# Performance work log

Hardware: AMD Instinct MI355X
Metric: run time of the kernel (lower is better)

The kernel has to match this reference:

```python
import jax, jax.numpy as jnp
import numpy as np


def setup_inputs() -> dict:
    key = jax.random.key(0)
    ks = jax.random.split(key, 6)
    B, H, W, Cin, Cout, wdim = 8, 64, 64, 512, 512, 512
    return {
        "x": jax.random.normal(ks[0], (B, H, W, Cin), jnp.float32),
        "w": jax.random.normal(ks[1], (B, wdim), jnp.float32),
        "noise": jax.random.normal(ks[2], (B, H, W, 1), jnp.float32),
        "style_weight": jax.random.normal(ks[3], (wdim, Cin), jnp.float32),
        "style_bias": jnp.ones((Cin,), jnp.float32),
        "conv_weight": jax.random.normal(ks[4], (3, 3, Cin, Cout), jnp.float32),
        "scale_noise": 0.1 * jax.random.normal(ks[5], (1, 1, 1, Cout), jnp.float32),
        "bias": jax.random.normal(jax.random.fold_in(key, 7), (Cout,), jnp.float32),
    }


def reference(x, w, noise, style_weight, style_bias, conv_weight, scale_noise, bias):
    wdim = style_weight.shape[0]
    kh, kw, cin, cout = conv_weight.shape
    # Equalized-LR fully connected to_style (gain=1, lr_mult=1, bias init ones,
    # activation=True -> leaky_relu(0.2) with sqrt(2) gain, StyleGAN2 convention).
    s = w @ (style_weight * (1.0 / np.sqrt(wdim))) + style_bias  # [B, Cin]
    s = jax.nn.leaky_relu(s, 0.2) * np.sqrt(2.0).astype(np.float32)
    # Modulated conv (demodulated). Equalized-LR weight scale 1/sqrt(fan_in).
    wk = conv_weight * (1.0 / np.sqrt(kh * kw * cin))  # [3,3,Cin,Cout]
    # demod[b,o] = rsqrt(sum_{h,w,i} (wk[h,w,i,o]*s[b,i])^2 + eps)
    d = jax.lax.rsqrt(jnp.einsum('hwio,bi->bo', wk * wk, s * s) + 1e-8)  # [B,Cout]
    xm = x * s[:, None, None, :]  # modulate inputs instead of per-sample weights
    y = jax.lax.conv_general_dilated(
        xm, wk, window_strides=(1, 1), padding='SAME',
        dimension_numbers=('NHWC', 'HWIO', 'NHWC'))
    y = y * d[:, None, None, :]
    # noise scale-add + bias + leaky-relu (the fused tail in StyleGAN2 kernels)
    y = y + scale_noise * noise + bias
    return jax.nn.leaky_relu(y, 0.2)
```

## Files before the change

### kernel.cpp

```cpp
#include <hip/hip_runtime.h>
#include <hip/hip_bf16.h>
#include <stdint.h>


typedef __attribute__((ext_vector_type(8))) __bf16 bf16x8;
typedef __attribute__((ext_vector_type(16))) float f32x16;

__device__ __forceinline__ float bf2f(ushort u) {
    union { uint32_t i; float f; } v; v.i = (uint32_t)u << 16; return v.f;
}
__device__ __forceinline__ ushort f2bf(float f) {
    union { float f; uint32_t i; } v; v.f = f;
    uint32_t r = v.i + 0x7fffu + ((v.i >> 16) & 1u);
    return (ushort)(r >> 16);
}
__device__ __forceinline__ int sniff_f32(const void* sb) {
    return ((const uint32_t*)sb)[0] == 0x3F800000u;
}
__device__ __forceinline__ float lda(const void* p, int idx, int isf) {
    return isf ? ((const float*)p)[idx] : bf2f(((const ushort*)p)[idx]);
}

union U16x8 { uint4 v; ushort u[8]; };

#define INV_SQRT_WDIM 0.04419417382415922f
#define SQRT2         1.4142135623730951f
#define WSCALE        0.014731391274719739f

__global__ void k_style_part(const void* __restrict__ w, const void* __restrict__ sw,
                             const void* __restrict__ sb, float* __restrict__ part) {
    int isf = sniff_f32(sb);
    int b = blockIdx.x >> 3, ds = blockIdx.x & 7;
    int i = threadIdx.x;
    __shared__ float wrow[64];
    if (i < 64) wrow[i] = lda(w, b * 512 + ds * 64 + i, isf);
    __syncthreads();
    float acc = 0.f;
    if (isf) {
        const float* p = (const float*)sw + (size_t)ds * 64 * 512;
#pragma unroll 8
        for (int d = 0; d < 64; ++d) acc += wrow[d] * p[d * 512 + i];
    } else {
        const ushort* p = (const ushort*)sw + (size_t)ds * 64 * 512;
#pragma unroll 8
        for (int d = 0; d < 64; ++d) acc += wrow[d] * bf2f(p[d * 512 + i]);
    }
    part[(b * 8 + ds) * 512 + i] = acc;
}

__global__ void k_style_fin(const float* __restrict__ part, const void* __restrict__ sb,
                            float* __restrict__ s_out) {
    int isf = sniff_f32(sb);
    int b = blockIdx.x, i = threadIdx.x;
    float a = 0.f;
#pragma unroll
    for (int ds = 0; ds < 8; ++ds) a += part[(b * 8 + ds) * 512 + i];
    float s = a * INV_SQRT_WDIM + lda(sb, i, isf);
    s = (s > 0.f ? s : 0.2f * s) * SQRT2;
    s_out[b * 512 + i] = s;
}

__global__ void k_pad(const void* __restrict__ x, const float* __restrict__ s,
                      const void* __restrict__ sb, ushort* __restrict__ xmp) {
    int isf = sniff_f32(sb);
    int pr = blockIdx.x;
    int b = pr / 66, yp = pr % 66;
    int tid = threadIdx.x;
    ushort* rowp = xmp + ((size_t)b * 66 + yp) * 66 * 512;
    uint4 z = {0u, 0u, 0u, 0u};
    if (yp == 0 || yp == 65) {
        uint4* p = (uint4*)rowp;
        for (int l = tid; l < 66 * 512 * 2 / 16; l += 256) p[l] = z;
        return;
    }
    __shared__ float sv[512];
    for (int c = tid; c < 512; c += 256) sv[c] = s[b * 512 + c];
    if (tid < 64)       ((uint4*)rowp)[tid] = z;
    else if (tid < 128) ((uint4*)(rowp + 65 * 512))[tid - 64] = z;
    __syncthreads();
    int y = yp - 1;
    ushort* xout = rowp + 512;
    if (isf) {
        const float* xin = (const float*)x + ((size_t)b * 64 + y) * 64 * 512;
        for (int l = tid; l < 8192; l += 256) {
            int xi = l >> 7, cc = (l & 127) * 4;
            float4 in = *(const float4*)(xin + (size_t)xi * 512 + cc);
            ushort4 ov;
            ov.x = f2bf(in.x * sv[cc + 0]);
            ov.y = f2bf(in.y * sv[cc + 1]);
            ov.z = f2bf(in.z * sv[cc + 2]);
            ov.w = f2bf(in.w * sv[cc + 3]);
            *(ushort4*)(xout + (size_t)xi * 512 + cc) = ov;
        }
    } else {
        const ushort* xin = (const ushort*)x + ((size_t)b * 64 + y) * 64 * 512;
        for (int l = tid; l < 4096; l += 256) {
            int xi = l >> 6, cc = (l & 63) * 8;
            U16x8 in, ov;
            in.v = *(const uint4*)(xin + (size_t)xi * 512 + cc);
#pragma unroll
            for (int j = 0; j < 8; ++j) ov.u[j] = f2bf(bf2f(in.u[j]) * sv[cc + j]);
            *(uint4*)(xout + (size_t)xi * 512 + cc) = ov.v;
        }
    }
}

__global__ void k_wt(const void* __restrict__ cw, const void* __restrict__ sb,
                     ushort* __restrict__ wkt) {
    int isf = sniff_f32(sb);
    int bid = blockIdx.x;
    int t = bid / 64, ib = (bid % 64) / 8, ob = bid % 8;
    __shared__ ushort tile[64][65];
    int tid = threadIdx.x;
    int oq = tid & 15, ir = tid >> 4;
#pragma unroll
    for (int p = 0; p < 4; ++p) {
        int i = p * 16 + ir;
        size_t off = ((size_t)(t * 512 + ib * 64 + i)) * 512 + ob * 64 + oq * 4;
        float v0, v1, v2, v3;
        if (isf) {
            float4 v = *(const float4*)((const float*)cw + off);
            v0 = v.x; v1 = v.y; v2 = v.z; v3 = v.w;
        } else {
            ushort4 v = *(const ushort4*)((const ushort*)cw + off);
            v0 = bf2f(v.x); v1 = bf2f(v.y); v2 = bf2f(v.z); v3 = bf2f(v.w);
        }
        tile[i][oq * 4 + 0] = f2bf(v0 * WSCALE);
        tile[i][oq * 4 + 1] = f2bf(v1 * WSCALE);
        tile[i][oq * 4 + 2] = f2bf(v2 * WSCALE);
        tile[i][oq * 4 + 3] = f2bf(v3 * WSCALE);
    }
    __syncthreads();
    int iq = tid & 15, orow = tid >> 4;
#pragma unroll
    for (int p = 0; p < 4; ++p) {
        int o = p * 16 + orow;
        ushort4 v;
        v.x = tile[iq * 4 + 0][o];
        v.y = tile[iq * 4 + 1][o];
        v.z = tile[iq * 4 + 2][o];
        v.w = tile[iq * 4 + 3][o];
        *(ushort4*)(wkt + ((size_t)(t * 512 + ob * 64 + o)) * 512 + ib * 64 + iq * 4) = v;
    }
}

__global__ void k_dmod(const ushort* __restrict__ wkt, const float* __restrict__ s,
                       float* __restrict__ part) {
    int t = blockIdx.x / 8, ob = blockIdx.x % 8;
    int tid = threadIdx.x;
    __shared__ float s2[4096];
    __shared__ float red[2048];
#pragma unroll
    for (int j = 0; j < 16; ++j) {
        int idx = j * 256 + tid;
        float v = s[idx];
        s2[idx] = v * v;
    }
    __syncthreads();
    int ol = tid >> 2, ks = tid & 3;
    int o = ob * 64 + ol;
    const ushort* row = wkt + (size_t)(t * 512 + o) * 512 + ks * 128;
    float acc[8] = {0, 0, 0, 0, 0, 0, 0, 0};
    for (int ch = 0; ch < 16; ++ch) {
        U16x8 wv; wv.v = *(const uint4*)(row + ch * 8);
        int ibase = ks * 128 + ch * 8;
#pragma unroll
        for (int e = 0; e < 8; ++e) {
            float wf = bf2f(wv.u[e]);
            float w2 = wf * wf;
#pragma unroll
            for (int b = 0; b < 8; ++b) acc[b] += w2 * s2[b * 512 + ibase + e];
        }
    }
#pragma unroll
    for (int b = 0; b < 8; ++b) red[(ol * 8 + b) * 4 + ks] = acc[b];
    __syncthreads();
#pragma unroll
    for (int p = 0; p < 2; ++p) {
        int q = tid * 2 + p;
        int ol2 = q >> 3, b2 = q & 7;
        float sum = red[q * 4 + 0] + red[q * 4 + 1] + red[q * 4 + 2] + red[q * 4 + 3];
        part[(b2 * 9 + t) * 512 + ob * 64 + ol2] = sum;
    }
}

__global__ void k_dfin(const float* __restrict__ part, float* __restrict__ d) {
    int gid = blockIdx.x * 256 + threadIdx.x;
    int b = gid >> 9, o = gid & 511;
    float acc = 1e-8f;
#pragma unroll
    for (int t = 0; t < 9; ++t) acc += part[(b * 9 + t) * 512 + o];
    d[b * 512 + o] = rsqrtf(acc);
}

#define GLL(gp, lp) __builtin_amdgcn_global_load_lds( \
    (const __attribute__((address_space(1))) void*)(gp), \
    (__attribute__((address_space(3))) void*)(lp), 16, 0, 0)

__launch_bounds__(256, 2)
__global__ void k_conv(const ushort* __restrict__ xmp, const ushort* __restrict__ wkt,
                       const float* __restrict__ dmod, const void* __restrict__ noise,
                       const void* __restrict__ snoise, const void* __restrict__ bias_,
                       const void* __restrict__ sb, void* __restrict__ out) {
    __shared__ ushort Ah[4 * 66 * 64];
    __shared__ ushort Bl[2][128 * 64];
    int isf = sniff_f32(sb);
    int id = blockIdx.x;
    int ct = id & 3;
    int rt = (id >> 2) & 31;
    int b  = id >> 7;
    int y0 = rt * 2, o0 = ct * 128;
    int tid = threadIdx.x;
    int lane = tid & 63, wv = tid >> 6;
    int wm = (wv >> 1) * 64, wn = (wv & 1) * 64;
    int lm = lane & 31, kh = lane >> 5;
    const ushort* xb = xmp + (size_t)b * 66 * 66 * 512;
    const ushort* wkt_o0 = wkt + (size_t)o0 * 512;

    f32x16 acc[2][2] = {};

    auto stageA = [&](int c0a) {
#pragma unroll
        for (int it = 0; it < 8; ++it) {
            int L = it * 256 + tid;
            int cidx = L >> 3, slot = L & 7;
            int hrow = cidx / 66, col = cidx - hrow * 66;
            int kc = slot ^ (col & 7);
            GLL(xb + ((size_t)(y0 + hrow) * 66 + col) * 512 + c0a + kc * 8,
                (char*)Ah + L * 16);
        }
        if (wv == 0) {
            int L = 2048 + tid;
            int cidx = L >> 3, slot = L & 7;
            int hrow = cidx / 66, col = cidx - hrow * 66;
            int kc = slot ^ (col & 7);
            GLL(xb + ((size_t)(y0 + hrow) * 66 + col) * 512 + c0a + kc * 8,
                (char*)Ah + L * 16);
        }
    };
    auto stageB = [&](int tap, int c0b, char* dst) {
#pragma unroll
        for (int it = 0; it < 4; ++it) {
            int L = it * 256 + tid;
            int row = L >> 3, slot = L & 7;
            int kc = slot ^ (row & 7);
            GLL(wkt_o0 + (size_t)tap * 262144 + (size_t)row * 512 + c0b + kc * 8,
                dst + L * 16);
        }
    };

    stageB(0, 0, (char*)Bl[0]);
    int u = 0;
    for (int c = 0; c < 8; ++c) {
        int c0 = c * 64;
        if (c) __syncthreads();
        stageA(c0);
        __syncthreads();
        for (int t = 0; t < 9; ++t, ++u) {
            if (t < 8)      stageB(t + 1, c0, (char*)Bl[(u + 1) & 1]);
            else if (c < 7) stageB(0, c0 + 64, (char*)Bl[(u + 1) & 1]);
            int dy = t / 3 - 1, dx = t % 3 - 1;
            int hrow = (wv >> 1) + dy + 1;
            const char* bb = (const char*)Bl[u & 1];
#pragma unroll
            for (int ks = 0; ks < 4; ++ks) {
                int ck = ks * 2 + kh;
                bf16x8 afr[2], bfr[2];
#pragma unroll
                for (int am = 0; am < 2; ++am) {
                    int col = am * 32 + lm + dx + 1;
                    afr[am] = *(const bf16x8*)((const char*)Ah +
                        (((hrow * 66 + col) << 3) + (ck ^ (col & 7))) * 16);
                }
#pragma unroll
                for (int bn = 0; bn < 2; ++bn) {
                    int row = wn + bn * 32 + lm;
                    bfr[bn] = *(const bf16x8*)(bb +
                        ((row << 3) + (ck ^ (row & 7))) * 16);
                }
#pragma unroll
                for (int am = 0; am < 2; ++am)
#pragma unroll
                    for (int bn = 0; bn < 2; ++bn)
                        acc[am][bn] = __builtin_amdgcn_mfma_f32_32x32x16_bf16(
                            afr[am], bfr[bn], acc[am][bn], 0, 0, 0);
            }
            __syncthreads();
        }
    }

    float dv[2], snv[2], bv[2];
#pragma unroll
    for (int bn = 0; bn < 2; ++bn) {
        int o = o0 + wn + bn * 32 + lm;
        dv[bn] = dmod[b * 512 + o];
        snv[bn] = lda(snoise, o, isf);
        bv[bn] = lda(bias_, o, isf);
    }
#pragma unroll
    for (int am = 0; am < 2; ++am) {
#pragma unroll
        for (int reg = 0; reg < 16; ++reg) {
            int p = wm + am * 32 + 4 * kh + (reg & 3) + 8 * (reg >> 2);
            int yy = y0 + (p >> 6), xx = p & 63;
            float nz = lda(noise, (b * 64 + yy) * 64 + xx, isf);
            size_t obase = ((size_t)(b * 64 + yy) * 64 + xx) * 512;
            if (isf) {
                float* of = (float*)out;
#pragma unroll
                for (int bn = 0; bn < 2; ++bn) {
                    float v = acc[am][bn][reg] * dv[bn] + snv[bn] * nz + bv[bn];
                    v = v > 0.f ? v : 0.2f * v;
                    of[obase + o0 + wn + bn * 32 + lm] = v;
                }
            } else {
                ushort* ob = (ushort*)out;
#pragma unroll
                for (int bn = 0; bn < 2; ++bn) {
                    float v = acc[am][bn][reg] * dv[bn] + snv[bn] * nz + bv[bn];
                    v = v > 0.f ? v : 0.2f * v;
                    ob[obase + o0 + wn + bn * 32 + lm] = f2bf(v);
                }
            }
        }
    }
}

extern "C" void kernel_launch(void* const* d_in, const int* in_sizes, int n_in,
                              void* d_out, int out_size, void* d_ws, size_t ws_size,
                              hipStream_t stream) {
    const void* x     = d_in[0];
    const void* w     = d_in[1];
    const void* noise = d_in[2];
    const void* sw    = d_in[3];
    const void* sb    = d_in[4];
    const void* cw    = d_in[5];
    const void* sn    = d_in[6];
    const void* bias  = d_in[7];

    char* ws = (char*)d_ws;
    ushort* xmp   = (ushort*)(ws);
    ushort* wkt   = (ushort*)(ws + 35684352);
    float*  s     = (float*)(ws + 40402944);
    float*  dmod  = (float*)(ws + 40419328);
    float*  part  = (float*)(ws + 40435712);
    float*  spart = (float*)(ws + 40583168);
    (void)in_sizes; (void)n_in; (void)out_size; (void)ws_size;

    hipLaunchKernelGGL(k_style_part, dim3(64),     dim3(512), 0, stream, w, sw, sb, spart);
    hipLaunchKernelGGL(k_style_fin,  dim3(8),      dim3(512), 0, stream, spart, sb, s);
    hipLaunchKernelGGL(k_wt,         dim3(576),    dim3(256), 0, stream, cw, sb, wkt);
    hipLaunchKernelGGL(k_dmod,       dim3(72),     dim3(256), 0, stream, wkt, s, part);
    hipLaunchKernelGGL(k_dfin,       dim3(16),     dim3(256), 0, stream, part, dmod);
    hipLaunchKernelGGL(k_pad,        dim3(8 * 66), dim3(256), 0, stream, x, s, sb, xmp);
    hipLaunchKernelGGL(k_conv,       dim3(1024),   dim3(256), 0, stream,
                       xmp, wkt, dmod, noise, sn, bias, sb, d_out);
}
```

Before: 339.2 us.

## Load conv weights directly into registers with fragment-friendly layout, double-buffer activations

Rewrites the weight transpose to a layout where each MFMA B-fragment is a contiguous 16-byte chunk, so the conv kernel loads weights straight from global memory into registers with a one-tap-ahead register prefetch instead of staging them through LDS. The freed LDS double-buffers the activation tile so the next channel chunk loads during compute, which removes the per-tap barriers. The demodulation kernel is adapted to the new weight layout. This costs more VGPRs for the register prefetch buffers, and B reads now go through L2 per wave with no LDS sharing across waves.

```diff
diff --git a/kernel.cpp b/kernel.cpp
--- a/kernel.cpp
+++ b/kernel.cpp
@@ -106,7 +106,7 @@
 }
 
 __global__ void k_wt(const void* __restrict__ cw, const void* __restrict__ sb,
-                     ushort* __restrict__ wkt) {
+                     ushort* __restrict__ wkt2) {
     int isf = sniff_f32(sb);
     int bid = blockIdx.x;
     int t = bid / 64, ib = (bid % 64) / 8, ob = bid % 8;
@@ -131,20 +131,20 @@
         tile[i][oq * 4 + 3] = f2bf(v3 * WSCALE);
     }
     __syncthreads();
-    int iq = tid & 15, orow = tid >> 4;
-#pragma unroll
-    for (int p = 0; p < 4; ++p) {
-        int o = p * 16 + orow;
-        ushort4 v;
-        v.x = tile[iq * 4 + 0][o];
-        v.y = tile[iq * 4 + 1][o];
-        v.z = tile[iq * 4 + 2][o];
-        v.w = tile[iq * 4 + 3][o];
-        *(ushort4*)(wkt + ((size_t)(t * 512 + ob * 64 + o)) * 512 + ib * 64 + iq * 4) = v;
-    }
-}
-
-__global__ void k_dmod(const ushort* __restrict__ wkt, const float* __restrict__ s,
+    int kql = tid >> 6, ol = tid & 63;
+    int kq = ib * 4 + kql;
+    U16x8 lo, hi;
+#pragma unroll
+    for (int j = 0; j < 8; ++j) {
+        lo.u[j] = tile[kql * 16 + j][ol];
+        hi.u[j] = tile[kql * 16 + 8 + j][ol];
+    }
+    uint4* dst = (uint4*)(wkt2 + ((size_t)((t * 32 + kq) * 512) + ob * 64 + ol) * 16);
+    dst[0] = lo.v;
+    dst[1] = hi.v;
+}
+
+__global__ void k_dmod(const ushort* __restrict__ wkt2, const float* __restrict__ s,
                        float* __restrict__ part) {
     int t = blockIdx.x / 8, ob = blockIdx.x % 8;
     int tid = threadIdx.x;
@@ -157,29 +157,39 @@
         s2[idx] = v * v;
     }
     __syncthreads();
-    int ol = tid >> 2, ks = tid & 3;
+    int q = tid >> 6, ol = tid & 63;
     int o = ob * 64 + ol;
-    const ushort* row = wkt + (size_t)(t * 512 + o) * 512 + ks * 128;
     float acc[8] = {0, 0, 0, 0, 0, 0, 0, 0};
-    for (int ch = 0; ch < 16; ++ch) {
-        U16x8 wv; wv.v = *(const uint4*)(row + ch * 8);
-        int ibase = ks * 128 + ch * 8;
+    for (int kk = 0; kk < 8; ++kk) {
+        int kq = q * 8 + kk;
+        const uint4* p = (const uint4*)(wkt2 + ((size_t)((t * 32 + kq) * 512) + o) * 16);
+        U16x8 w0, w1;
+        w0.v = p[0];
+        w1.v = p[1];
+        int ibase = kq * 16;
 #pragma unroll
         for (int e = 0; e < 8; ++e) {
-            float wf = bf2f(wv.u[e]);
+            float wf = bf2f(w0.u[e]);
             float w2 = wf * wf;
 #pragma unroll
             for (int b = 0; b < 8; ++b) acc[b] += w2 * s2[b * 512 + ibase + e];
         }
-    }
-#pragma unroll
-    for (int b = 0; b < 8; ++b) red[(ol * 8 + b) * 4 + ks] = acc[b];
+#pragma unroll
+        for (int e = 0; e < 8; ++e) {
+            float wf = bf2f(w1.u[e]);
+            float w2 = wf * wf;
+#pragma unroll
+            for (int b = 0; b < 8; ++b) acc[b] += w2 * s2[b * 512 + ibase + 8 + e];
+        }
+    }
+#pragma unroll
+    for (int b = 0; b < 8; ++b) red[(ol * 8 + b) * 4 + q] = acc[b];
     __syncthreads();
 #pragma unroll
     for (int p = 0; p < 2; ++p) {
-        int q = tid * 2 + p;
-        int ol2 = q >> 3, b2 = q & 7;
-        float sum = red[q * 4 + 0] + red[q * 4 + 1] + red[q * 4 + 2] + red[q * 4 + 3];
+        int qq = tid * 2 + p;
+        int ol2 = qq >> 3, b2 = qq & 7;
+        float sum = red[qq * 4 + 0] + red[qq * 4 + 1] + red[qq * 4 + 2] + red[qq * 4 + 3];
         part[(b2 * 9 + t) * 512 + ob * 64 + ol2] = sum;
     }
 }
@@ -198,12 +208,11 @@
     (__attribute__((address_space(3))) void*)(lp), 16, 0, 0)
 
 __launch_bounds__(256, 2)
-__global__ void k_conv(const ushort* __restrict__ xmp, const ushort* __restrict__ wkt,
+__global__ void k_conv(const ushort* __restrict__ xmp, const ushort* __restrict__ wkt2,
                        const float* __restrict__ dmod, const void* __restrict__ noise,
                        const void* __restrict__ snoise, const void* __restrict__ bias_,
                        const void* __restrict__ sb, void* __restrict__ out) {
-    __shared__ ushort Ah[4 * 66 * 64];
-    __shared__ ushort Bl[2][128 * 64];
+    __shared__ ushort Ah[2][4 * 66 * 64];
     int isf = sniff_f32(sb);
     int id = blockIdx.x;
     int ct = id & 3;
@@ -215,11 +224,13 @@
     int wm = (wv >> 1) * 64, wn = (wv & 1) * 64;
     int lm = lane & 31, kh = lane >> 5;
     const ushort* xb = xmp + (size_t)b * 66 * 66 * 512;
-    const ushort* wkt_o0 = wkt + (size_t)o0 * 512;
+    const char* bp = (const char*)wkt2;
+    size_t boff = ((size_t)(o0 + wn + lm)) * 32 + (size_t)(kh * 16);
 
     f32x16 acc[2][2] = {};
-
-    auto stageA = [&](int c0a) {
+    bf16x8 bA[2][4], bB[2][4];
+
+    auto stageA = [&](int c0a, char* dstA) {
 #pragma unroll
         for (int it = 0; it < 8; ++it) {
             int L = it * 256 + tid;
@@ -227,7 +238,7 @@
             int hrow = cidx / 66, col = cidx - hrow * 66;
             int kc = slot ^ (col & 7);
             GLL(xb + ((size_t)(y0 + hrow) * 66 + col) * 512 + c0a + kc * 8,
-                (char*)Ah + L * 16);
+                dstA + L * 16);
         }
         if (wv == 0) {
             int L = 2048 + tid;
@@ -235,58 +246,65 @@
             int hrow = cidx / 66, col = cidx - hrow * 66;
             int kc = slot ^ (col & 7);
             GLL(xb + ((size_t)(y0 + hrow) * 66 + col) * 512 + c0a + kc * 8,
-                (char*)Ah + L * 16);
+                dstA + L * 16);
         }
     };
-    auto stageB = [&](int tap, int c0b, char* dst) {
-#pragma unroll
-        for (int it = 0; it < 4; ++it) {
-            int L = it * 256 + tid;
-            int row = L >> 3, slot = L & 7;
-            int kc = slot ^ (row & 7);
-            GLL(wkt_o0 + (size_t)tap * 262144 + (size_t)row * 512 + c0b + kc * 8,
-                dst + L * 16);
+
+    auto loadB = [&](int tt, int cc, bf16x8 (&dst)[2][4]) {
+#pragma unroll
+        for (int ks = 0; ks < 4; ++ks) {
+            int kq = cc * 4 + ks;
+            const char* pk = bp + (size_t)(tt * 32 + kq) * 16384 + boff;
+            dst[0][ks] = *(const bf16x8*)(pk);
+            dst[1][ks] = *(const bf16x8*)(pk + 1024);
         }
     };
 
-    stageB(0, 0, (char*)Bl[0]);
-    int u = 0;
+    auto tap = [&](int t, const bf16x8 (&cur)[2][4], bf16x8 (&nxt)[2][4],
+                   int pre_t, int pre_c, const char* AhC) {
+        if (pre_t >= 0) loadB(pre_t, pre_c, nxt);
+        int dy = t / 3 - 1, dx = t % 3 - 1;
+        int hrow = (wv >> 1) + dy + 1;
+#pragma unroll
+        for (int ks = 0; ks < 4; ++ks) {
+            int ck = ks * 2 + kh;
+            bf16x8 afr[2];
+#pragma unroll
+            for (int am = 0; am < 2; ++am) {
+                int col = am * 32 + lm + dx + 1;
+                afr[am] = *(const bf16x8*)(AhC +
+                    (((hrow * 66 + col) << 3) + (ck ^ (col & 7))) * 16);
+            }
+#pragma unroll
+            for (int am = 0; am < 2; ++am)
+#pragma unroll
+                for (int bn = 0; bn < 2; ++bn)
+                    acc[am][bn] = __builtin_amdgcn_mfma_f32_32x32x16_bf16(
+                        afr[am], cur[bn][ks], acc[am][bn], 0, 0, 0);
+        }
+    };
+
+    stageA(0, (char*)Ah[0]);
+    loadB(0, 0, bA);
+    __syncthreads();
     for (int c = 0; c < 8; ++c) {
-        int c0 = c * 64;
-        if (c) __syncthreads();
-        stageA(c0);
+        if (c < 7) stageA((c + 1) * 64, (char*)Ah[(c + 1) & 1]);
+        const char* AhC = (const char*)Ah[c & 1];
+        tap(0, bA, bB, 1, c, AhC);
+        tap(1, bB, bA, 2, c, AhC);
+        tap(2, bA, bB, 3, c, AhC);
+        tap(3, bB, bA, 4, c, AhC);
+        tap(4, bA, bB, 5, c, AhC);
+        tap(5, bB, bA, 6, c, AhC);
+        tap(6, bA, bB, 7, c, AhC);
+        tap(7, bB, bA, 8, c, AhC);
+        tap(8, bA, bB, (c < 7) ? 0 : -1, c + 1, AhC);
+#pragma unroll
+        for (int ks = 0; ks < 4; ++ks) {
+            bA[0][ks] = bB[0][ks];
+            bA[1][ks] = bB[1][ks];
+        }
         __syncthreads();
-        for (int t = 0; t < 9; ++t, ++u) {
-            if (t < 8)      stageB(t + 1, c0, (char*)Bl[(u + 1) & 1]);
-            else if (c < 7) stageB(0, c0 + 64, (char*)Bl[(u + 1) & 1]);
-            int dy = t / 3 - 1, dx = t % 3 - 1;
-            int hrow = (wv >> 1) + dy + 1;
-            const char* bb = (const char*)Bl[u & 1];
-#pragma unroll
-            for (int ks = 0; ks < 4; ++ks) {
-                int ck = ks * 2 + kh;
-                bf16x8 afr[2], bfr[2];
-#pragma unroll
-                for (int am = 0; am < 2; ++am) {
-                    int col = am * 32 + lm + dx + 1;
-                    afr[am] = *(const bf16x8*)((const char*)Ah +
-                        (((hrow * 66 + col) << 3) + (ck ^ (col & 7))) * 16);
-                }
-#pragma unroll
-                for (int bn = 0; bn < 2; ++bn) {
-                    int row = wn + bn * 32 + lm;
-                    bfr[bn] = *(const bf16x8*)(bb +
-                        ((row << 3) + (ck ^ (row & 7))) * 16);
-                }
-#pragma unroll
-                for (int am = 0; am < 2; ++am)
-#pragma unroll
-                    for (int bn = 0; bn < 2; ++bn)
-                        acc[am][bn] = __builtin_amdgcn_mfma_f32_32x32x16_bf16(
-                            afr[am], bfr[bn], acc[am][bn], 0, 0, 0);
-            }
-            __syncthreads();
-        }
     }
 
     float dv[2], snv[2], bv[2];
@@ -340,7 +358,7 @@
 
     char* ws = (char*)d_ws;
     ushort* xmp   = (ushort*)(ws);
-    ushort* wkt   = (ushort*)(ws + 35684352);
+    ushort* wkt2  = (ushort*)(ws + 35684352);
     float*  s     = (float*)(ws + 40402944);
     float*  dmod  = (float*)(ws + 40419328);
     float*  part  = (float*)(ws + 40435712);
@@ -349,10 +367,10 @@
 
     hipLaunchKernelGGL(k_style_part, dim3(64),     dim3(512), 0, stream, w, sw, sb, spart);
     hipLaunchKernelGGL(k_style_fin,  dim3(8),      dim3(512), 0, stream, spart, sb, s);
-    hipLaunchKernelGGL(k_wt,         dim3(576),    dim3(256), 0, stream, cw, sb, wkt);
-    hipLaunchKernelGGL(k_dmod,       dim3(72),     dim3(256), 0, stream, wkt, s, part);
+    hipLaunchKernelGGL(k_wt,         dim3(576),    dim3(256), 0, stream, cw, sb, wkt2);
+    hipLaunchKernelGGL(k_dmod,       dim3(72),     dim3(256), 0, stream, wkt2, s, part);
     hipLaunchKernelGGL(k_dfin,       dim3(16),     dim3(256), 0, stream, part, dmod);
     hipLaunchKernelGGL(k_pad,        dim3(8 * 66), dim3(256), 0, stream, x, s, sb, xmp);
     hipLaunchKernelGGL(k_conv,       dim3(1024),   dim3(256), 0, stream,
-                       xmp, wkt, dmod, noise, sn, bias, sb, d_out);
-}
+                       xmp, wkt2, dmod, noise, sn, bias, sb, d_out);
+}
```

Result: no change. 341.3 us (+0.6%).
